# Kernel tuning notes

Measured on AMD Instinct MI355X. Metric: run time of the kernel, lower is better.

## Reference

```python
import jax, jax.numpy as jnp
import numpy as np

WS = 7            # window_size
N = WS * WS       # tokens per window = 49
DIM = 128
H = 4             # num_heads
HD = DIM // H     # head_dim = 32
BNW = 8192        # batch * num_windows
NW = 64           # windows per image (for the shift mask)


def _relative_position_index(ws):
    # standard Swin relative position index, computed in numpy (static)
    coords = np.stack(np.meshgrid(np.arange(ws), np.arange(ws), indexing='ij'))  # [2,ws,ws]
    coords = coords.reshape(2, -1)                      # [2, N]
    rel = coords[:, :, None] - coords[:, None, :]       # [2, N, N]
    rel = rel.transpose(1, 2, 0)                        # [N, N, 2]
    rel[:, :, 0] += ws - 1
    rel[:, :, 1] += ws - 1
    rel[:, :, 0] *= 2 * ws - 1
    return rel.sum(-1).astype(np.int32)                 # [N, N] in [0, (2ws-1)^2)


def setup_inputs() -> dict:
    key = jax.random.key(0)
    ks = jax.random.split(key, 7)
    x = jax.random.normal(ks[0], (BNW, N, DIM), dtype=jnp.float32)
    # shifted-window mask: 0 where tokens may attend, -100 where blocked
    m = jax.random.uniform(ks[1], (NW, N, N))
    attn_mask = jnp.where(m < 0.9, 0.0, -100.0).astype(jnp.float32)
    qkv_w = jax.random.normal(ks[2], (3 * DIM, DIM), dtype=jnp.float32) * (DIM ** -0.5)
    qkv_b = jax.random.normal(ks[3], (3 * DIM,), dtype=jnp.float32) * 0.02
    proj_w = jax.random.normal(ks[4], (DIM, DIM), dtype=jnp.float32) * (DIM ** -0.5)
    proj_b = jax.random.normal(ks[5], (DIM,), dtype=jnp.float32) * 0.02
    rpb_table = jax.random.normal(ks[6], ((2 * WS - 1) ** 2, H), dtype=jnp.float32) * 0.02
    rpb_index = jnp.asarray(_relative_position_index(WS))
    return {"x": x, "attn_mask": attn_mask, "qkv_w": qkv_w, "qkv_b": qkv_b,
            "proj_w": proj_w, "proj_b": proj_b, "rpb_table": rpb_table,
            "rpb_index": rpb_index}


def reference(x, attn_mask, qkv_w, qkv_b, proj_w, proj_b, rpb_table, rpb_index):
    Bnw, n, c = x.shape
    scale = HD ** -0.5
    # QKV projection: [Bnw, N, 3*C] -> [3, Bnw, H, N, HD]
    qkv = (x @ qkv_w.T + qkv_b).reshape(Bnw, n, 3, H, HD)
    q = qkv[:, :, 0].transpose(0, 2, 1, 3)  # [Bnw, H, N, HD]
    k = qkv[:, :, 1].transpose(0, 2, 1, 3)
    v = qkv[:, :, 2].transpose(0, 2, 1, 3)
    attn = jnp.einsum('bhnd,bhmd->bhnm', q, k) * scale    # [Bnw, H, N, N]
    # relative position bias: [N,N] index into [169,H] table -> [H,N,N]
    bias = rpb_table[rpb_index.reshape(-1)].reshape(n, n, H).transpose(2, 0, 1)
    attn = attn + bias[None]
    # shift mask: broadcast over batch groups of nW windows
    nW = attn_mask.shape[0]
    attn = attn.reshape(-1, nW, H, n, n) + attn_mask[None, :, None]
    attn = attn.reshape(-1, H, n, n)
    attn = jax.nn.softmax(attn, axis=-1)
    y = jnp.einsum('bhnm,bhmd->bhnd', attn, v)            # [Bnw, H, N, HD]
    y = y.transpose(0, 2, 1, 3).reshape(Bnw, n, c)
    return y @ proj_w.T + proj_b
```

## Files before the change

### kernel.cpp

```cpp
#include <hip/hip_runtime.h>
#include <hip/hip_bf16.h>

#define NTOK 49
#define DIM  128
#define NH   4
#define HD   32
#define NWIN 8192
#define NWM  64

typedef short short8 __attribute__((ext_vector_type(8)));
typedef float f32x4  __attribute__((ext_vector_type(4)));

__device__ __forceinline__ short f2bf(float f) {
  return __builtin_bit_cast(short, __float2bfloat16(f));
}

__global__ void prep_weights(const float* __restrict__ qkv_w,
                             const float* __restrict__ proj_w,
                             short* __restrict__ wq, short* __restrict__ wp) {
  int i = blockIdx.x * 256 + threadIdx.x;
  if (i < 3 * DIM * DIM) wq[i] = f2bf(qkv_w[i]);
  else wp[i - 3 * DIM * DIM] = f2bf(proj_w[i - 3 * DIM * DIM]);
}

__global__ void prep_bm(const float* __restrict__ attn_mask,
                        const float* __restrict__ rpb_table,
                        const int* __restrict__ rpb_index,
                        float* __restrict__ bm) {
  int wm = blockIdx.x >> 2, h = blockIdx.x & 3;
  const float* mrow = attn_mask + wm * (NTOK * NTOK);
  float* dst = bm + blockIdx.x * (NTOK * NTOK);
  for (int i = threadIdx.x; i < NTOK * NTOK; i += 256)
    dst[i] = rpb_table[rpb_index[i] * NH + h] + mrow[i];
}

#define A_BASE 0
#define Q_BASE 16384
#define K_BASE 32768
#define LDS_BYTES 49152

__device__ __forceinline__ int aswz(int row, int slot) {
  return row * 256 + (((slot ^ (row & 7)) & 15) << 4);
}
__device__ __forceinline__ int qkswz(int m, int slot) {
  return m * 64 + (((slot ^ ((m >> 1) & 3)) & 3) << 4);
}
__device__ __forceinline__ int pvswz(int m, int slot) {
  return m * 128 + (((slot ^ (m & 7)) & 7) << 4);
}

template<bool USE_BM>
__global__ void __launch_bounds__(256, 3)
swin_attn(const float* __restrict__ x,
          const short* __restrict__ wq, const short* __restrict__ wp,
          const float* __restrict__ qkv_b, const float* __restrict__ proj_b,
          const float* __restrict__ bm,
          const int* __restrict__ rpb_index, const float* __restrict__ rpb_table,
          const float* __restrict__ attn_mask,
          float* __restrict__ out) {
  __shared__ __align__(16) char smem[LDS_BYTES];
  const int w    = blockIdx.x;
  const int tid  = threadIdx.x;
  const int h    = tid >> 6;
  const int lane = tid & 63;
  const int l16  = lane & 15;
  const int quad = lane >> 4;

  char* ab = smem + A_BASE;
  char* qh = smem + Q_BASE + h * 4096;
  char* kh = smem + K_BASE + h * 4096;
  char* vb = smem + A_BASE + h * 4096;
  char* yb = smem + K_BASE;
  char* plo = qh;
  char* phi = kh - 32 * 128;

  const float* xw = x + (size_t)w * (NTOK * DIM);
  #pragma unroll
  for (int it = 0; it < 4; ++it) {
    int u = tid + it * 256;
    if (u < NTOK * 16) {
      int row = u >> 4, c8 = u & 15;
      const f32x4* p = (const f32x4*)(xw + row * DIM + c8 * 8);
      f32x4 f0 = p[0], f1 = p[1];
      short8 a;
      a[0]=f2bf(f0[0]); a[1]=f2bf(f0[1]); a[2]=f2bf(f0[2]); a[3]=f2bf(f0[3]);
      a[4]=f2bf(f1[0]); a[5]=f2bf(f1[1]); a[6]=f2bf(f1[2]); a[7]=f2bf(f1[3]);
      *(short8*)(ab + aswz(row, c8)) = a;
    }
  }
  __syncthreads();

  const float scale = 0.17677669529663687f;

  #pragma unroll
  for (int c = 0; c < 3; ++c) {
    const int o0 = c * DIM + h * HD;
    f32x4 acc[2][4];
    #pragma unroll
    for (int nt = 0; nt < 2; ++nt)
      #pragma unroll
      for (int mt = 0; mt < 4; ++mt) { f32x4 z = {0.f,0.f,0.f,0.f}; acc[nt][mt] = z; }
    #pragma unroll
    for (int ks = 0; ks < 4; ++ks) {
      short8 b0 = *(const short8*)(wq + (o0 + l16) * DIM + ks * 32 + quad * 8);
      short8 b1 = *(const short8*)(wq + (o0 + 16 + l16) * DIM + ks * 32 + quad * 8);
      short8 aA[4];
      #pragma unroll
      for (int mt = 0; mt < 4; ++mt) {
        int row = mt * 16 + l16; if (row > 48) row = 48;
        aA[mt] = *(const short8*)(ab + aswz(row, ks * 4 + quad));
      }
      #pragma unroll
      for (int mt = 0; mt < 4; ++mt) {
        acc[0][mt] = __builtin_amdgcn_mfma_f32_16x16x32_bf16(aA[mt], b0, acc[0][mt], 0, 0, 0);
        acc[1][mt] = __builtin_amdgcn_mfma_f32_16x16x32_bf16(aA[mt], b1, acc[1][mt], 0, 0, 0);
      }
    }
    if (c == 2) __syncthreads();
    #pragma unroll
    for (int nt = 0; nt < 2; ++nt) {
      float bias = qkv_b[o0 + nt * 16 + l16];
      #pragma unroll
      for (int mt = 0; mt < 4; ++mt)
        #pragma unroll
        for (int r = 0; r < 4; ++r) {
          int m = mt * 16 + quad * 4 + r;
          int d = nt * 16 + l16;
          float v = acc[nt][mt][r] + bias;
          if (c == 0)      *(short*)(qh + qkswz(m, d >> 3) + (d & 7) * 2) = f2bf(v * scale);
          else if (c == 1) *(short*)(kh + qkswz(m, d >> 3) + (d & 7) * 2) = f2bf(v);
          else             *(short*)(vb + pvswz(d, m >> 3) + (m & 7) * 2) = f2bf(v);
        }
    }
  }

  f32x4 s[4][4];
  #pragma unroll
  for (int mt = 0; mt < 4; ++mt)
    #pragma unroll
    for (int nt = 0; nt < 4; ++nt) { f32x4 z = {0.f,0.f,0.f,0.f}; s[mt][nt] = z; }
  {
    short8 aQ[4], bK[4];
    #pragma unroll
    for (int mt = 0; mt < 4; ++mt)
      aQ[mt] = *(const short8*)(qh + qkswz(mt * 16 + l16, quad));
    #pragma unroll
    for (int nt = 0; nt < 4; ++nt)
      bK[nt] = *(const short8*)(kh + qkswz(nt * 16 + l16, quad));
    #pragma unroll
    for (int mt = 0; mt < 4; ++mt)
      #pragma unroll
      for (int nt = 0; nt < 4; ++nt)
        s[mt][nt] = __builtin_amdgcn_mfma_f32_16x16x32_bf16(aQ[mt], bK[nt], s[mt][nt], 0, 0, 0);
  }

  const int wm = w & (NWM - 1);
  const float* bmh = USE_BM ? bm + (size_t)(wm * NH + h) * (NTOK * NTOK) : nullptr;
  float rinv[4][4];
  #pragma unroll
  for (int mt = 0; mt < 4; ++mt) {
    char* pbase = (mt < 2) ? plo : phi;
    #pragma unroll
    for (int r = 0; r < 4; ++r) {
      int m = mt * 16 + quad * 4 + r;
      #pragma unroll
      for (int nt = 0; nt < 4; ++nt) {
        int n = nt * 16 + l16;
        float v = s[mt][nt][r];
        if (n >= NTOK) v = -1e30f;
        else if (m < NTOK) {
          if (USE_BM) v += bmh[m * NTOK + n];
          else v += rpb_table[rpb_index[m * NTOK + n] * NH + h]
                  + attn_mask[(wm * NTOK + m) * NTOK + n];
        }
        s[mt][nt][r] = v;
      }
      float mx = fmaxf(fmaxf(s[mt][0][r], s[mt][1][r]), fmaxf(s[mt][2][r], s[mt][3][r]));
      mx = fmaxf(mx, __shfl_xor(mx, 1, 16));
      mx = fmaxf(mx, __shfl_xor(mx, 2, 16));
      mx = fmaxf(mx, __shfl_xor(mx, 4, 16));
      mx = fmaxf(mx, __shfl_xor(mx, 8, 16));
      float t = 0.f;
      #pragma unroll
      for (int nt = 0; nt < 4; ++nt) {
        float p = __expf(s[mt][nt][r] - mx);
        s[mt][nt][r] = p;
        t += p;
      }
      t += __shfl_xor(t, 1, 16);
      t += __shfl_xor(t, 2, 16);
      t += __shfl_xor(t, 4, 16);
      t += __shfl_xor(t, 8, 16);
      rinv[mt][r] = __builtin_amdgcn_rcpf(t);
      #pragma unroll
      for (int nt = 0; nt < 4; ++nt) {
        int n = nt * 16 + l16;
        *(short*)(pbase + pvswz(m, n >> 3) + (n & 7) * 2) = f2bf(s[mt][nt][r]);
      }
    }
  }

  f32x4 y[2][4];
  #pragma unroll
  for (int dt = 0; dt < 2; ++dt)
    #pragma unroll
    for (int mt = 0; mt < 4; ++mt) { f32x4 z = {0.f,0.f,0.f,0.f}; y[dt][mt] = z; }
  #pragma unroll
  for (int kt = 0; kt < 2; ++kt) {
    short8 aP[4], bV[2];
    #pragma unroll
    for (int mt = 0; mt < 4; ++mt) {
      char* pbase = (mt < 2) ? plo : phi;
      aP[mt] = *(const short8*)(pbase + pvswz(mt * 16 + l16, kt * 4 + quad));
    }
    #pragma unroll
    for (int dt = 0; dt < 2; ++dt)
      bV[dt] = *(const short8*)(vb + pvswz(dt * 16 + l16, kt * 4 + quad));
    #pragma unroll
    for (int dt = 0; dt < 2; ++dt)
      #pragma unroll
      for (int mt = 0; mt < 4; ++mt)
        y[dt][mt] = __builtin_amdgcn_mfma_f32_16x16x32_bf16(aP[mt], bV[dt], y[dt][mt], 0, 0, 0);
  }
  #pragma unroll
  for (int dt = 0; dt < 2; ++dt)
    #pragma unroll
    for (int mt = 0; mt < 4; ++mt)
      #pragma unroll
      for (int r = 0; r < 4; ++r)
        y[dt][mt][r] *= rinv[mt][r];

  __syncthreads();
  #pragma unroll
  for (int dt = 0; dt < 2; ++dt)
    #pragma unroll
    for (int mt = 0; mt < 4; ++mt)
      #pragma unroll
      for (int r = 0; r < 4; ++r) {
        int m = mt * 16 + quad * 4 + r;
        int e = h * HD + dt * 16 + l16;
        *(short*)(yb + aswz(m, e >> 3) + (e & 7) * 2) = f2bf(y[dt][mt][r]);
      }
  __syncthreads();

  {
    const int o0 = h * 32;
    f32x4 oa[2][4];
    #pragma unroll
    for (int nt = 0; nt < 2; ++nt)
      #pragma unroll
      for (int mt = 0; mt < 4; ++mt) { f32x4 z = {0.f,0.f,0.f,0.f}; oa[nt][mt] = z; }
    #pragma unroll
    for (int ks = 0; ks < 4; ++ks) {
      short8 aY[4];
      #pragma unroll
      for (int mt = 0; mt < 4; ++mt)
        aY[mt] = *(const short8*)(yb + aswz(mt * 16 + l16, ks * 4 + quad));
      short8 b0 = *(const short8*)(wp + (o0 + l16) * DIM + ks * 32 + quad * 8);
      short8 b1 = *(const short8*)(wp + (o0 + 16 + l16) * DIM + ks * 32 + quad * 8);
      #pragma unroll
      for (int mt = 0; mt < 4; ++mt) {
        oa[0][mt] = __builtin_amdgcn_mfma_f32_16x16x32_bf16(aY[mt], b0, oa[0][mt], 0, 0, 0);
        oa[1][mt] = __builtin_amdgcn_mfma_f32_16x16x32_bf16(aY[mt], b1, oa[1][mt], 0, 0, 0);
      }
    }
    float pb0 = proj_b[o0 + l16], pb1 = proj_b[o0 + 16 + l16];
    float* ow = out + (size_t)w * (NTOK * DIM);
    #pragma unroll
    for (int nt = 0; nt < 2; ++nt) {
      float pbv = nt ? pb1 : pb0;
      #pragma unroll
      for (int mt = 0; mt < 4; ++mt)
        #pragma unroll
        for (int r = 0; r < 4; ++r) {
          int m = mt * 16 + quad * 4 + r;
          if (m < NTOK) ow[m * DIM + o0 + nt * 16 + l16] = oa[nt][mt][r] + pbv;
        }
    }
  }
}

extern "C" void kernel_launch(void* const* d_in, const int* in_sizes, int n_in,
                              void* d_out, int out_size, void* d_ws, size_t ws_size,
                              hipStream_t stream) {
  const float* x         = (const float*)d_in[0];
  const float* attn_mask = (const float*)d_in[1];
  const float* qkv_w     = (const float*)d_in[2];
  const float* qkv_b     = (const float*)d_in[3];
  const float* proj_w    = (const float*)d_in[4];
  const float* proj_b    = (const float*)d_in[5];
  const float* rpb_table = (const float*)d_in[6];
  const int*   rpb_index = (const int*)d_in[7];
  float* out = (float*)d_out;

  short* wq = (short*)d_ws;
  short* wp = wq + 3 * DIM * DIM;
  float* bmp = (float*)((char*)d_ws + 131072);
  size_t need = 131072 + (size_t)NWM * NH * NTOK * NTOK * sizeof(float);

  prep_weights<<<256, 256, 0, stream>>>(qkv_w, proj_w, wq, wp);
  if (ws_size >= need) {
    prep_bm<<<256, 256, 0, stream>>>(attn_mask, rpb_table, rpb_index, bmp);
    swin_attn<true><<<NWIN, 256, 0, stream>>>(x, wq, wp, qkv_b, proj_b, bmp,
                                              rpb_index, rpb_table, attn_mask, out);
  } else {
    swin_attn<false><<<NWIN, 256, 0, stream>>>(x, wq, wp, qkv_b, proj_b, nullptr,
                                               rpb_index, rpb_table, attn_mask, out);
  }
}
```

Baseline: 529.7 us.

## Permute LDS layouts to pack bf16 stores and use DPP row reductions

Q, K, P and Y tiles are written to LDS in a permuted column order, so each lane writes packed 2- or 4-element bf16 vectors instead of scalar shorts. The proj weight is pre-permuted in the prep kernel to match the new Y column order, and V's token dimension is permuted the same way as P's. Softmax row max and sum reductions now use DPP row-shuffle instructions instead of __shfl_xor. The aim is fewer LDS store instructions and cheaper cross-lane reductions, at the cost of consistent permutations across several stages that must all line up to stay correct.

After: 504.3 us. -4.8%, faster.

```diff
diff --git a/kernel.cpp b/kernel.cpp
--- a/kernel.cpp
+++ b/kernel.cpp
@@ -9,18 +9,29 @@
 #define NWM  64
 
 typedef short short8 __attribute__((ext_vector_type(8)));
+typedef short short4v __attribute__((ext_vector_type(4)));
+typedef short short2v __attribute__((ext_vector_type(2)));
 typedef float f32x4  __attribute__((ext_vector_type(4)));
 
 __device__ __forceinline__ short f2bf(float f) {
   return __builtin_bit_cast(short, __float2bfloat16(f));
 }
+
+#define DPPF(x, ctrl) __builtin_bit_cast(float, __builtin_amdgcn_update_dpp( \
+    0, __builtin_bit_cast(int, (x)), (ctrl), 0xf, 0xf, true))
 
 __global__ void prep_weights(const float* __restrict__ qkv_w,
                              const float* __restrict__ proj_w,
                              short* __restrict__ wq, short* __restrict__ wp) {
   int i = blockIdx.x * 256 + threadIdx.x;
-  if (i < 3 * DIM * DIM) wq[i] = f2bf(qkv_w[i]);
-  else wp[i - 3 * DIM * DIM] = f2bf(proj_w[i - 3 * DIM * DIM]);
+  if (i < 3 * DIM * DIM) {
+    wq[i] = f2bf(qkv_w[i]);
+  } else {
+    int j = i - 3 * DIM * DIM;
+    int o = j >> 7, e = j & 127;
+    int ep = (e & 96) + ((e & 15) << 1) + ((e >> 4) & 1);
+    wp[o * DIM + ep] = f2bf(proj_w[j]);
+  }
 }
 
 __global__ void prep_bm(const float* __restrict__ attn_mask,
@@ -39,14 +50,14 @@
 #define K_BASE 32768
 #define LDS_BYTES 49152
 
-__device__ __forceinline__ int aswz(int row, int slot) {
-  return row * 256 + (((slot ^ (row & 7)) & 15) << 4);
-}
-__device__ __forceinline__ int qkswz(int m, int slot) {
-  return m * 64 + (((slot ^ ((m >> 1) & 3)) & 3) << 4);
-}
-__device__ __forceinline__ int pvswz(int m, int slot) {
-  return m * 128 + (((slot ^ (m & 7)) & 7) << 4);
+__device__ __forceinline__ int a_byte(int row, int cb) {
+  return row * 256 + ((((cb >> 4) ^ (row & 7)) & 15) << 4) + (cb & 15);
+}
+__device__ __forceinline__ int qk_byte(int row, int cb) {
+  return row * 64 + ((((cb >> 4) ^ ((row >> 1) & 3)) & 3) << 4) + (cb & 15);
+}
+__device__ __forceinline__ int pv_byte(int row, int cb) {
+  return row * 128 + ((((cb >> 4) ^ (row & 7)) & 7) << 4) + (cb & 15);
 }
 
 template<bool USE_BM>
@@ -85,7 +96,7 @@
       short8 a;
       a[0]=f2bf(f0[0]); a[1]=f2bf(f0[1]); a[2]=f2bf(f0[2]); a[3]=f2bf(f0[3]);
       a[4]=f2bf(f1[0]); a[5]=f2bf(f1[1]); a[6]=f2bf(f1[2]); a[7]=f2bf(f1[3]);
-      *(short8*)(ab + aswz(row, c8)) = a;
+      *(short8*)(ab + a_byte(row, c8 * 16)) = a;
     }
   }
   __syncthreads();
@@ -108,7 +119,7 @@
       #pragma unroll
       for (int mt = 0; mt < 4; ++mt) {
         int row = mt * 16 + l16; if (row > 48) row = 48;
-        aA[mt] = *(const short8*)(ab + aswz(row, ks * 4 + quad));
+        aA[mt] = *(const short8*)(ab + a_byte(row, (ks * 4 + quad) * 16));
       }
       #pragma unroll
       for (int mt = 0; mt < 4; ++mt) {
@@ -117,19 +128,27 @@
       }
     }
     if (c == 2) __syncthreads();
-    #pragma unroll
-    for (int nt = 0; nt < 2; ++nt) {
-      float bias = qkv_b[o0 + nt * 16 + l16];
+    {
+      float bias0 = qkv_b[o0 + l16];
+      float bias1 = qkv_b[o0 + 16 + l16];
       #pragma unroll
       for (int mt = 0; mt < 4; ++mt)
         #pragma unroll
         for (int r = 0; r < 4; ++r) {
           int m = mt * 16 + quad * 4 + r;
-          int d = nt * 16 + l16;
-          float v = acc[nt][mt][r] + bias;
-          if (c == 0)      *(short*)(qh + qkswz(m, d >> 3) + (d & 7) * 2) = f2bf(v * scale);
-          else if (c == 1) *(short*)(kh + qkswz(m, d >> 3) + (d & 7) * 2) = f2bf(v);
-          else             *(short*)(vb + pvswz(d, m >> 3) + (m & 7) * 2) = f2bf(v);
+          float v0 = acc[0][mt][r] + bias0;
+          float v1 = acc[1][mt][r] + bias1;
+          if (c == 0) {
+            short2v pk; pk[0] = f2bf(v0 * scale); pk[1] = f2bf(v1 * scale);
+            *(short2v*)(qh + qk_byte(m, l16 * 4)) = pk;
+          } else if (c == 1) {
+            short2v pk; pk[0] = f2bf(v0); pk[1] = f2bf(v1);
+            *(short2v*)(kh + qk_byte(m, l16 * 4)) = pk;
+          } else {
+            int cb = (((m & 15) << 2) | (m >> 4)) * 2;
+            *(short*)(vb + pv_byte(l16,      cb)) = f2bf(v0);
+            *(short*)(vb + pv_byte(l16 + 16, cb)) = f2bf(v1);
+          }
         }
     }
   }
@@ -143,10 +162,10 @@
     short8 aQ[4], bK[4];
     #pragma unroll
     for (int mt = 0; mt < 4; ++mt)
-      aQ[mt] = *(const short8*)(qh + qkswz(mt * 16 + l16, quad));
+      aQ[mt] = *(const short8*)(qh + qk_byte(mt * 16 + l16, quad * 16));
     #pragma unroll
     for (int nt = 0; nt < 4; ++nt)
-      bK[nt] = *(const short8*)(kh + qkswz(nt * 16 + l16, quad));
+      bK[nt] = *(const short8*)(kh + qk_byte(nt * 16 + l16, quad * 16));
     #pragma unroll
     for (int mt = 0; mt < 4; ++mt)
       #pragma unroll
@@ -176,10 +195,10 @@
         s[mt][nt][r] = v;
       }
       float mx = fmaxf(fmaxf(s[mt][0][r], s[mt][1][r]), fmaxf(s[mt][2][r], s[mt][3][r]));
-      mx = fmaxf(mx, __shfl_xor(mx, 1, 16));
-      mx = fmaxf(mx, __shfl_xor(mx, 2, 16));
-      mx = fmaxf(mx, __shfl_xor(mx, 4, 16));
-      mx = fmaxf(mx, __shfl_xor(mx, 8, 16));
+      mx = fmaxf(mx, DPPF(mx, 0x121));
+      mx = fmaxf(mx, DPPF(mx, 0x122));
+      mx = fmaxf(mx, DPPF(mx, 0x124));
+      mx = fmaxf(mx, DPPF(mx, 0x128));
       float t = 0.f;
       #pragma unroll
       for (int nt = 0; nt < 4; ++nt) {
@@ -187,16 +206,15 @@
         s[mt][nt][r] = p;
         t += p;
       }
-      t += __shfl_xor(t, 1, 16);
-      t += __shfl_xor(t, 2, 16);
-      t += __shfl_xor(t, 4, 16);
-      t += __shfl_xor(t, 8, 16);
+      t += DPPF(t, 0x121);
+      t += DPPF(t, 0x122);
+      t += DPPF(t, 0x124);
+      t += DPPF(t, 0x128);
       rinv[mt][r] = __builtin_amdgcn_rcpf(t);
-      #pragma unroll
-      for (int nt = 0; nt < 4; ++nt) {
-        int n = nt * 16 + l16;
-        *(short*)(pbase + pvswz(m, n >> 3) + (n & 7) * 2) = f2bf(s[mt][nt][r]);
-      }
+      short4v pk;
+      pk[0] = f2bf(s[mt][0][r]); pk[1] = f2bf(s[mt][1][r]);
+      pk[2] = f2bf(s[mt][2][r]); pk[3] = f2bf(s[mt][3][r]);
+      *(short4v*)(pbase + pv_byte(m, l16 << 3)) = pk;
     }
   }
 
@@ -211,11 +229,11 @@
     #pragma unroll
     for (int mt = 0; mt < 4; ++mt) {
       char* pbase = (mt < 2) ? plo : phi;
-      aP[mt] = *(const short8*)(pbase + pvswz(mt * 16 + l16, kt * 4 + quad));
+      aP[mt] = *(const short8*)(pbase + pv_byte(mt * 16 + l16, (kt * 4 + quad) * 16));
     }
     #pragma unroll
     for (int dt = 0; dt < 2; ++dt)
-      bV[dt] = *(const short8*)(vb + pvswz(dt * 16 + l16, kt * 4 + quad));
+      bV[dt] = *(const short8*)(vb + pv_byte(dt * 16 + l16, (kt * 4 + quad) * 16));
     #pragma unroll
     for (int dt = 0; dt < 2; ++dt)
       #pragma unroll
@@ -232,15 +250,13 @@
 
   __syncthreads();
   #pragma unroll
-  for (int dt = 0; dt < 2; ++dt)
-    #pragma unroll
-    for (int mt = 0; mt < 4; ++mt)
-      #pragma unroll
-      for (int r = 0; r < 4; ++r) {
-        int m = mt * 16 + quad * 4 + r;
-        int e = h * HD + dt * 16 + l16;
-        *(short*)(yb + aswz(m, e >> 3) + (e & 7) * 2) = f2bf(y[dt][mt][r]);
-      }
+  for (int mt = 0; mt < 4; ++mt)
+    #pragma unroll
+    for (int r = 0; r < 4; ++r) {
+      int m = mt * 16 + quad * 4 + r;
+      short2v pk; pk[0] = f2bf(y[0][mt][r]); pk[1] = f2bf(y[1][mt][r]);
+      *(short2v*)(yb + a_byte(m, h * 64 + l16 * 4)) = pk;
+    }
   __syncthreads();
 
   {
@@ -255,7 +271,7 @@
       short8 aY[4];
       #pragma unroll
       for (int mt = 0; mt < 4; ++mt)
-        aY[mt] = *(const short8*)(yb + aswz(mt * 16 + l16, ks * 4 + quad));
+        aY[mt] = *(const short8*)(yb + a_byte(mt * 16 + l16, (ks * 4 + quad) * 16));
       short8 b0 = *(const short8*)(wp + (o0 + l16) * DIM + ks * 32 + quad * 8);
       short8 b1 = *(const short8*)(wp + (o0 + 16 + l16) * DIM + ks * 32 + quad * 8);
       #pragma unroll
```
